# Kernel optimization log

Hardware: AMD Instinct MI355X
Metric: run time of the kernel (lower is better)

## Reference

```python
import jax, jax.numpy as jnp
import numpy as np

N, DIM, K = 262144, 64, 1024

def setup_inputs() -> dict:
    key = jax.random.key(0)
    k1, k2 = jax.random.split(key)
    x = jax.random.normal(k1, (N, DIM), dtype=jnp.float32)
    embed = jax.random.normal(k2, (K, DIM), dtype=jnp.float32)
    return {"x": x, "embed": embed}

def reference(x, embed):
    distances = (jnp.sum(x * x, axis=-1, keepdims=True)
                 - 2.0 * (x @ embed.T)
                 + jnp.sum(embed * embed, axis=-1))  # [N, K]
    idx = jnp.argmin(distances, axis=-1)  # [N]
    # dequantize: embedding lookup
    out = embed[idx]  # [N, DIM]
    return out
```

## Files before the change

kernel.cpp:

```cpp
#include <hip/hip_runtime.h>


#define VQ_N 262144
#define VQ_DIM 64
#define VQ_K 1024
#define NT 64
#define TCH 256
#define FLAG_EPS 1.2e-2f

typedef short short8 __attribute__((ext_vector_type(8)));
typedef float f32x4 __attribute__((ext_vector_type(4)));

#define WS_BFRAG 0
#define WS_E2    (256*1024)
#define WS_NEEDED (260*1024)

static __device__ __forceinline__ unsigned short f2bf_rtne(float f) {
    unsigned u = __float_as_uint(f);
    unsigned r = u + 0x7FFFu + ((u >> 16) & 1u);
    return (unsigned short)(r >> 16);
}
static __device__ __forceinline__ float bf2f(unsigned short h) {
    return __uint_as_float(((unsigned)h) << 16);
}

__global__ void vq_prep(const float* __restrict__ embed, unsigned char* ws) {
    int t = blockIdx.x * 256 + threadIdx.x;
    if (t < NT * TCH) {
        int ct = t >> 8;
        int c = t & 255;
        int arr = c >> 7;
        int kc = (c >> 6) & 1;
        int l = c & 63;
        int code = ct * 16 + (l & 15);
        int kbase = kc * 32 + ((l >> 4) << 3);
        const float* ep = embed + (size_t)code * VQ_DIM + kbase;
        short8 pack;
#pragma unroll
        for (int j = 0; j < 8; ++j) {
            float v = ep[j];
            unsigned short h = f2bf_rtne(v);
            pack[j] = arr ? (short)f2bf_rtne(v - bf2f(h)) : (short)h;
        }
        ((short8*)(ws + WS_BFRAG))[t] = pack;
    } else if (t < NT * TCH + VQ_K) {
        int code = t - NT * TCH;
        const float* ep = embed + (size_t)code * VQ_DIM;
        float a0 = 0, a1 = 0, a2 = 0, a3 = 0;
#pragma unroll
        for (int j = 0; j < VQ_DIM; j += 4) {
            a0 = fmaf(ep[j], ep[j], a0);
            a1 = fmaf(ep[j + 1], ep[j + 1], a1);
            a2 = fmaf(ep[j + 2], ep[j + 2], a2);
            a3 = fmaf(ep[j + 3], ep[j + 3], a3);
        }
        ((float*)(ws + WS_E2))[code] = (a0 + a1) + (a2 + a3);
    }
}

__global__ __launch_bounds__(256, 2)
void vq_stage1(const float* __restrict__ x, const float* __restrict__ embed,
               unsigned char* ws, float* __restrict__ out) {
    __shared__ int idx_s[4][64];

    const int tid = threadIdx.x;
    const int lane = tid & 63;
    const int wave = tid >> 6;
    const int gwave = blockIdx.x * 4 + wave;
    const int R0 = gwave * 64;
    const int g = lane >> 4;
    const int khalf = g << 3;

    const short8* bsrc = (const short8*)(ws + WS_BFRAG);
    const float* e2g = (const float*)(ws + WS_E2);

    short8 ah00, ah01, al00, al01, ah10, ah11, al10, al11;
    short8 ah20, ah21, al20, al21, ah30, ah31, al30, al31;
#define MAKE_A(ROW, KC, AH, AL)                                             \
    {                                                                       \
        const float4* p4 = (const float4*)(x + (size_t)(ROW) * VQ_DIM +     \
                                           (KC) * 32 + khalf);              \
        float4 v0 = p4[0], v1 = p4[1];                                      \
        float q0 = -2.0f * v0.x, q1 = -2.0f * v0.y, q2 = -2.0f * v0.z,      \
              q3 = -2.0f * v0.w, q4 = -2.0f * v1.x, q5 = -2.0f * v1.y,      \
              q6 = -2.0f * v1.z, q7 = -2.0f * v1.w;                         \
        unsigned short h0 = f2bf_rtne(q0), h1 = f2bf_rtne(q1),              \
                       h2 = f2bf_rtne(q2), h3 = f2bf_rtne(q3),              \
                       h4 = f2bf_rtne(q4), h5 = f2bf_rtne(q5),              \
                       h6 = f2bf_rtne(q6), h7 = f2bf_rtne(q7);              \
        AH[0] = (short)h0; AH[1] = (short)h1; AH[2] = (short)h2;            \
        AH[3] = (short)h3; AH[4] = (short)h4; AH[5] = (short)h5;            \
        AH[6] = (short)h6; AH[7] = (short)h7;                               \
        AL[0] = (short)f2bf_rtne(q0 - bf2f(h0));                            \
        AL[1] = (short)f2bf_rtne(q1 - bf2f(h1));                            \
        AL[2] = (short)f2bf_rtne(q2 - bf2f(h2));                            \
        AL[3] = (short)f2bf_rtne(q3 - bf2f(h3));                            \
        AL[4] = (short)f2bf_rtne(q4 - bf2f(h4));                            \
        AL[5] = (short)f2bf_rtne(q5 - bf2f(h5));                            \
        AL[6] = (short)f2bf_rtne(q6 - bf2f(h6));                            \
        AL[7] = (short)f2bf_rtne(q7 - bf2f(h7));                            \
    }
    const int rowb = R0 + (lane & 15);
    MAKE_A(rowb +  0, 0, ah00, al00)  MAKE_A(rowb +  0, 1, ah01, al01)
    MAKE_A(rowb + 16, 0, ah10, al10)  MAKE_A(rowb + 16, 1, ah11, al11)
    MAKE_A(rowb + 32, 0, ah20, al20)  MAKE_A(rowb + 32, 1, ah21, al21)
    MAKE_A(rowb + 48, 0, ah30, al30)  MAKE_A(rowb + 48, 1, ah31, al31)
#undef MAKE_A

    unsigned m1k0[4], m2k0[4], m1k1[4], m2k1[4];
    unsigned m1k2[4], m2k2[4], m1k3[4], m2k3[4];
#pragma unroll
    for (int r = 0; r < 4; ++r) {
        m1k0[r] = 0xFFFFFFFFu; m2k0[r] = 0xFFFFFFFFu;
        m1k1[r] = 0xFFFFFFFFu; m2k1[r] = 0xFFFFFFFFu;
        m1k2[r] = 0xFFFFFFFFu; m2k2[r] = 0xFFFFFFFFu;
        m1k3[r] = 0xFFFFFFFFu; m2k3[r] = 0xFFFFFFFFu;
    }

#define DO_SET(AH0, AH1, AL0, AL1, M1, M2)                                            \
    {                                                                                 \
        f32x4 acc = {e2c, e2c, e2c, e2c};                                             \
        acc = __builtin_amdgcn_mfma_f32_16x16x32_bf16(AL0, bh0, acc, 0, 0, 0);        \
        acc = __builtin_amdgcn_mfma_f32_16x16x32_bf16(AL1, bh1, acc, 0, 0, 0);        \
        acc = __builtin_amdgcn_mfma_f32_16x16x32_bf16(AH0, bl0, acc, 0, 0, 0);        \
        acc = __builtin_amdgcn_mfma_f32_16x16x32_bf16(AH1, bl1, acc, 0, 0, 0);        \
        acc = __builtin_amdgcn_mfma_f32_16x16x32_bf16(AH0, bh0, acc, 0, 0, 0);        \
        acc = __builtin_amdgcn_mfma_f32_16x16x32_bf16(AH1, bh1, acc, 0, 0, 0);        \
        _Pragma("unroll")                                                             \
        for (int r = 0; r < 4; ++r) {                                                 \
            unsigned key = (__float_as_uint(acc[r]) & 0xFFFFFFC0u) | ctu;             \
            unsigned t1 = M1[r] > key ? M1[r] : key;                                  \
            M2[r] = M2[r] < t1 ? M2[r] : t1;                                          \
            M1[r] = M1[r] < key ? M1[r] : key;                                        \
        }                                                                             \
    }

#pragma unroll 2
    for (int ct = 0; ct < NT; ++ct) {
        const short8* bt = bsrc + (size_t)ct * TCH;
        short8 bh0 = bt[lane];
        short8 bh1 = bt[64 + lane];
        short8 bl0 = bt[128 + lane];
        short8 bl1 = bt[192 + lane];
        float e2c = e2g[ct * 16 + (lane & 15)] + 256.0f;
        unsigned ctu = (unsigned)ct;

        DO_SET(ah00, ah01, al00, al01, m1k0, m2k0)
        DO_SET(ah10, ah11, al10, al11, m1k1, m2k1)
        DO_SET(ah20, ah21, al20, al21, m1k2, m2k2)
        DO_SET(ah30, ah31, al30, al31, m1k3, m2k3)
    }
#undef DO_SET

    unsigned res0[4], res1[4], res2[4], res3[4];
#pragma unroll
    for (int r = 0; r < 4; ++r) {
        res0[r] = (unsigned)(lane & 15); res1[r] = res0[r];
        res2[r] = res0[r]; res3[r] = res0[r];
    }
#define RED_STEP(M1, M2, RES, m)                                                      \
    {                                                                                 \
        _Pragma("unroll")                                                             \
        for (int r = 0; r < 4; ++r) {                                                 \
            unsigned ok = (unsigned)__shfl_xor((int)M1[r], m);                        \
            unsigned ok2 = (unsigned)__shfl_xor((int)M2[r], m);                       \
            unsigned orr = (unsigned)__shfl_xor((int)RES[r], m);                      \
            unsigned t1 = M1[r] > ok ? M1[r] : ok;                                    \
            unsigned c2 = ok2 < t1 ? ok2 : t1;                                        \
            M2[r] = M2[r] < c2 ? M2[r] : c2;                                          \
            bool take = (ok < M1[r]) || (ok == M1[r] && orr < RES[r]);                \
            if (take) { M1[r] = ok; RES[r] = orr; }                                   \
        }                                                                             \
    }
#pragma unroll
    for (int m = 1; m <= 8; m <<= 1) {
        RED_STEP(m1k0, m2k0, res0, m)
        RED_STEP(m1k1, m2k1, res1, m)
        RED_STEP(m1k2, m2k2, res2, m)
        RED_STEP(m1k3, m2k3, res3, m)
    }
#undef RED_STEP

    unsigned long long lmask = 0ull;
    if ((lane & 15) == 0) {
#define PUB(M1, M2, RES, SET)                                                         \
        _Pragma("unroll")                                                             \
        for (int r = 0; r < 4; ++r) {                                                 \
            int p = (SET) * 16 + 4 * g + r;                                           \
            idx_s[wave][p] = (int)((M1[r] & 63u) * 16u + RES[r]);                     \
            float s1 = __uint_as_float(M1[r] & 0xFFFFFFC0u);                          \
            float s2 = __uint_as_float(M2[r] & 0xFFFFFFC0u);                          \
            if (s2 - s1 < FLAG_EPS) lmask |= 1ull << p;                               \
        }
        PUB(m1k0, m2k0, res0, 0)
        PUB(m1k1, m2k1, res1, 1)
        PUB(m1k2, m2k2, res2, 2)
        PUB(m1k3, m2k3, res3, 3)
#undef PUB
    }
    lmask |= (unsigned long long)__shfl_xor((long long)lmask, 16);
    lmask |= (unsigned long long)__shfl_xor((long long)lmask, 32);
    unsigned long long wmask = (unsigned long long)__shfl((long long)lmask, 0);
    __syncthreads();

    const int chunk = tid & 15;
#pragma unroll
    for (int jj = 0; jj < 16; ++jj) {
        int rib = jj * 16 + (tid >> 4);
        int code = idx_s[rib >> 6][rib & 63];
        const float4* ep = (const float4*)(embed + (size_t)code * VQ_DIM) + chunk;
        float4* op = (float4*)(out + (size_t)(blockIdx.x * 256 + rib) * VQ_DIM) + chunk;
        *op = *ep;
    }
    __syncthreads();

    while (wmask) {
        int b = __ffsll((unsigned long long)wmask) - 1;
        wmask &= wmask - 1;
        int row = R0 + b;
        const float* xr = x + (size_t)row * VQ_DIM;
        float xv[VQ_DIM];
#pragma unroll
        for (int j = 0; j < VQ_DIM / 4; ++j) {
            float4 v = ((const float4*)xr)[j];
            xv[4 * j] = v.x; xv[4 * j + 1] = v.y;
            xv[4 * j + 2] = v.z; xv[4 * j + 3] = v.w;
        }
        float best = __builtin_inff();
        int bi = VQ_K;
        for (int t = 0; t < VQ_K / 64; ++t) {
            int c = t * 64 + lane;
            const float* ep = embed + (size_t)c * VQ_DIM;
            float a0 = 0, a1 = 0, a2 = 0, a3 = 0;
#pragma unroll
            for (int j = 0; j < VQ_DIM; j += 4) {
                a0 = fmaf(xv[j], ep[j], a0);
                a1 = fmaf(xv[j + 1], ep[j + 1], a1);
                a2 = fmaf(xv[j + 2], ep[j + 2], a2);
                a3 = fmaf(xv[j + 3], ep[j + 3], a3);
            }
            float dot = (a0 + a1) + (a2 + a3);
            float s = fmaf(-2.0f, dot, e2g[c]);
            if (s < best || (s == best && c < bi)) { best = s; bi = c; }
        }
#pragma unroll
        for (int m = 1; m <= 32; m <<= 1) {
            float ob = __shfl_xor(best, m);
            int oi = __shfl_xor(bi, m);
            if (ob < best || (ob == best && oi < bi)) { best = ob; bi = oi; }
        }
        out[(size_t)row * VQ_DIM + lane] = embed[(size_t)bi * VQ_DIM + lane];
    }
}

__global__ __launch_bounds__(256, 4)
void vq_fallback(const float* __restrict__ x, const float* __restrict__ embed,
                 float* __restrict__ out) {
    __shared__ float e2s[VQ_K];
    const int tid = threadIdx.x;
    for (int c = tid; c < VQ_K; c += 256) {
        const float4* ep = (const float4*)(embed + c * VQ_DIM);
        float s = 0.0f;
#pragma unroll
        for (int j = 0; j < VQ_DIM / 4; ++j) {
            float4 v = ep[j];
            s = fmaf(v.x, v.x, s); s = fmaf(v.y, v.y, s);
            s = fmaf(v.z, v.z, s); s = fmaf(v.w, v.w, s);
        }
        e2s[c] = s;
    }
    __syncthreads();
    const int row = blockIdx.x * 256 + tid;
    float xr[VQ_DIM];
    const float4* xp = (const float4*)(x + (size_t)row * VQ_DIM);
#pragma unroll
    for (int j = 0; j < VQ_DIM / 4; ++j) {
        float4 v = xp[j];
        xr[4 * j] = v.x; xr[4 * j + 1] = v.y; xr[4 * j + 2] = v.z; xr[4 * j + 3] = v.w;
    }
    float best = __builtin_inff();
    int bidx = 0;
    for (int c = 0; c < VQ_K; ++c) {
        const float4* ep = (const float4*)(embed + c * VQ_DIM);
        float a0 = 0, a1 = 0, a2 = 0, a3 = 0;
#pragma unroll
        for (int j = 0; j < VQ_DIM / 4; ++j) {
            float4 v = ep[j];
            a0 = fmaf(xr[4 * j], v.x, a0);
            a1 = fmaf(xr[4 * j + 1], v.y, a1);
            a2 = fmaf(xr[4 * j + 2], v.z, a2);
            a3 = fmaf(xr[4 * j + 3], v.w, a3);
        }
        float score = fmaf(-2.0f, (a0 + a1) + (a2 + a3), e2s[c]);
        if (score < best) { best = score; bidx = c; }
    }
    const float4* bp = (const float4*)(embed + (size_t)bidx * VQ_DIM);
    float4* op = (float4*)(out + (size_t)row * VQ_DIM);
#pragma unroll
    for (int j = 0; j < VQ_DIM / 4; ++j) op[j] = bp[j];
}

extern "C" void kernel_launch(void* const* d_in, const int* in_sizes, int n_in,
                              void* d_out, int out_size, void* d_ws, size_t ws_size,
                              hipStream_t stream) {
    const float* x = (const float*)d_in[0];
    const float* embed = (const float*)d_in[1];
    float* out = (float*)d_out;
    if (ws_size < WS_NEEDED) {
        hipLaunchKernelGGL(vq_fallback, dim3(VQ_N / 256), dim3(256), 0, stream, x, embed, out);
        return;
    }
    unsigned char* ws = (unsigned char*)d_ws;
    hipLaunchKernelGGL(vq_prep, dim3(68), dim3(256), 0, stream, embed, ws);
    hipLaunchKernelGGL(vq_stage1, dim3(VQ_N / 256), dim3(256), 0, stream, x, embed, ws, out);
}
```

Before: 183.3 us.

## Halve rows per wave, double occupancy, prefetch codebook tiles with rotated start

```diff
diff --git a/kernel.cpp b/kernel.cpp
--- a/kernel.cpp
+++ b/kernel.cpp
@@ -13,7 +13,8 @@
 
 #define WS_BFRAG 0
 #define WS_E2    (256*1024)
-#define WS_NEEDED (260*1024)
+#define WS_E2P   (260*1024)
+#define WS_NEEDED (264*1024)
 
 static __device__ __forceinline__ unsigned short f2bf_rtne(float f) {
     unsigned u = __float_as_uint(f);
@@ -54,28 +55,30 @@
             a2 = fmaf(ep[j + 2], ep[j + 2], a2);
             a3 = fmaf(ep[j + 3], ep[j + 3], a3);
         }
-        ((float*)(ws + WS_E2))[code] = (a0 + a1) + (a2 + a3);
-    }
-}
-
-__global__ __launch_bounds__(256, 2)
+        float e2 = (a0 + a1) + (a2 + a3);
+        ((float*)(ws + WS_E2))[code] = e2;
+        ((float*)(ws + WS_E2P))[code] = e2 + 256.0f;
+    }
+}
+
+__global__ __launch_bounds__(256, 4)
 void vq_stage1(const float* __restrict__ x, const float* __restrict__ embed,
                unsigned char* ws, float* __restrict__ out) {
-    __shared__ int idx_s[4][64];
+    __shared__ int idx_s[4][32];
 
     const int tid = threadIdx.x;
     const int lane = tid & 63;
     const int wave = tid >> 6;
     const int gwave = blockIdx.x * 4 + wave;
-    const int R0 = gwave * 64;
+    const int R0 = gwave * 32;
     const int g = lane >> 4;
     const int khalf = g << 3;
 
     const short8* bsrc = (const short8*)(ws + WS_BFRAG);
     const float* e2g = (const float*)(ws + WS_E2);
+    const float* e2p = (const float*)(ws + WS_E2P);
 
     short8 ah00, ah01, al00, al01, ah10, ah11, al10, al11;
-    short8 ah20, ah21, al20, al21, ah30, ah31, al30, al31;
 #define MAKE_A(ROW, KC, AH, AL)                                             \
     {                                                                       \
         const float4* p4 = (const float4*)(x + (size_t)(ROW) * VQ_DIM +     \
@@ -100,32 +103,37 @@
         AL[6] = (short)f2bf_rtne(q6 - bf2f(h6));                            \
         AL[7] = (short)f2bf_rtne(q7 - bf2f(h7));                            \
     }
-    const int rowb = R0 + (lane & 15);
-    MAKE_A(rowb +  0, 0, ah00, al00)  MAKE_A(rowb +  0, 1, ah01, al01)
-    MAKE_A(rowb + 16, 0, ah10, al10)  MAKE_A(rowb + 16, 1, ah11, al11)
-    MAKE_A(rowb + 32, 0, ah20, al20)  MAKE_A(rowb + 32, 1, ah21, al21)
-    MAKE_A(rowb + 48, 0, ah30, al30)  MAKE_A(rowb + 48, 1, ah31, al31)
+    const int row0 = R0 + (lane & 15);
+    const int row1 = row0 + 16;
+    MAKE_A(row0, 0, ah00, al00)
+    MAKE_A(row0, 1, ah01, al01)
+    MAKE_A(row1, 0, ah10, al10)
+    MAKE_A(row1, 1, ah11, al11)
 #undef MAKE_A
 
     unsigned m1k0[4], m2k0[4], m1k1[4], m2k1[4];
-    unsigned m1k2[4], m2k2[4], m1k3[4], m2k3[4];
 #pragma unroll
     for (int r = 0; r < 4; ++r) {
         m1k0[r] = 0xFFFFFFFFu; m2k0[r] = 0xFFFFFFFFu;
         m1k1[r] = 0xFFFFFFFFu; m2k1[r] = 0xFFFFFFFFu;
-        m1k2[r] = 0xFFFFFFFFu; m2k2[r] = 0xFFFFFFFFu;
-        m1k3[r] = 0xFFFFFFFFu; m2k3[r] = 0xFFFFFFFFu;
-    }
-
-#define DO_SET(AH0, AH1, AL0, AL1, M1, M2)                                            \
+    }
+
+#define LOAD_B(CT, B0, B1, B2, B3)                                          \
+    {                                                                       \
+        const short8* bt = bsrc + (size_t)(CT) * TCH;                       \
+        B0 = bt[lane]; B1 = bt[64 + lane];                                  \
+        B2 = bt[128 + lane]; B3 = bt[192 + lane];                           \
+    }
+
+#define DO_SET(AH0, AH1, AL0, AL1, B0, B1, B2, B3, M1, M2)                            \
     {                                                                                 \
         f32x4 acc = {e2c, e2c, e2c, e2c};                                             \
-        acc = __builtin_amdgcn_mfma_f32_16x16x32_bf16(AL0, bh0, acc, 0, 0, 0);        \
-        acc = __builtin_amdgcn_mfma_f32_16x16x32_bf16(AL1, bh1, acc, 0, 0, 0);        \
-        acc = __builtin_amdgcn_mfma_f32_16x16x32_bf16(AH0, bl0, acc, 0, 0, 0);        \
-        acc = __builtin_amdgcn_mfma_f32_16x16x32_bf16(AH1, bl1, acc, 0, 0, 0);        \
-        acc = __builtin_amdgcn_mfma_f32_16x16x32_bf16(AH0, bh0, acc, 0, 0, 0);        \
-        acc = __builtin_amdgcn_mfma_f32_16x16x32_bf16(AH1, bh1, acc, 0, 0, 0);        \
+        acc = __builtin_amdgcn_mfma_f32_16x16x32_bf16(AL0, B0, acc, 0, 0, 0);         \
+        acc = __builtin_amdgcn_mfma_f32_16x16x32_bf16(AL1, B1, acc, 0, 0, 0);         \
+        acc = __builtin_amdgcn_mfma_f32_16x16x32_bf16(AH0, B2, acc, 0, 0, 0);         \
+        acc = __builtin_amdgcn_mfma_f32_16x16x32_bf16(AH1, B3, acc, 0, 0, 0);         \
+        acc = __builtin_amdgcn_mfma_f32_16x16x32_bf16(AH0, B0, acc, 0, 0, 0);         \
+        acc = __builtin_amdgcn_mfma_f32_16x16x32_bf16(AH1, B1, acc, 0, 0, 0);         \
         _Pragma("unroll")                                                             \
         for (int r = 0; r < 4; ++r) {                                                 \
             unsigned key = (__float_as_uint(acc[r]) & 0xFFFFFFC0u) | ctu;             \
@@ -135,29 +143,33 @@
         }                                                                             \
     }
 
-#pragma unroll 2
-    for (int ct = 0; ct < NT; ++ct) {
-        const short8* bt = bsrc + (size_t)ct * TCH;
-        short8 bh0 = bt[lane];
-        short8 bh1 = bt[64 + lane];
-        short8 bl0 = bt[128 + lane];
-        short8 bl1 = bt[192 + lane];
-        float e2c = e2g[ct * 16 + (lane & 15)] + 256.0f;
-        unsigned ctu = (unsigned)ct;
-
-        DO_SET(ah00, ah01, al00, al01, m1k0, m2k0)
-        DO_SET(ah10, ah11, al10, al11, m1k1, m2k1)
-        DO_SET(ah20, ah21, al20, al21, m1k2, m2k2)
-        DO_SET(ah30, ah31, al30, al31, m1k3, m2k3)
-    }
+#define DO_TILE(CT, B0, B1, B2, B3)                                                   \
+    {                                                                                 \
+        float e2c = e2p[(CT) * 16 + (lane & 15)];                                     \
+        unsigned ctu = (unsigned)(CT);                                                \
+        DO_SET(ah00, ah01, al00, al01, B0, B1, B2, B3, m1k0, m2k0)                    \
+        DO_SET(ah10, ah11, al10, al11, B0, B1, B2, B3, m1k1, m2k1)                    \
+    }
+
+    const int rot = gwave & 63;
+    short8 pb0, pb1, pb2, pb3, qb0, qb1, qb2, qb3;
+    LOAD_B(rot, pb0, pb1, pb2, pb3)
+    for (int it = 0; it < NT; it += 2) {
+        const int cte = (rot + it) & 63;
+        const int cto = (rot + it + 1) & 63;
+        const int ctn = (rot + it + 2) & 63;
+        LOAD_B(cto, qb0, qb1, qb2, qb3)
+        DO_TILE(cte, pb0, pb1, pb2, pb3)
+        LOAD_B(ctn, pb0, pb1, pb2, pb3)
+        DO_TILE(cto, qb0, qb1, qb2, qb3)
+    }
+#undef DO_TILE
 #undef DO_SET
-
-    unsigned res0[4], res1[4], res2[4], res3[4];
-#pragma unroll
-    for (int r = 0; r < 4; ++r) {
-        res0[r] = (unsigned)(lane & 15); res1[r] = res0[r];
-        res2[r] = res0[r]; res3[r] = res0[r];
-    }
+#undef LOAD_B
+
+    unsigned res0[4], res1[4];
+#pragma unroll
+    for (int r = 0; r < 4; ++r) { res0[r] = (unsigned)(lane & 15); res1[r] = res0[r]; }
 #define RED_STEP(M1, M2, RES, m)                                                      \
     {                                                                                 \
         _Pragma("unroll")                                                             \
@@ -176,46 +188,41 @@
     for (int m = 1; m <= 8; m <<= 1) {
         RED_STEP(m1k0, m2k0, res0, m)
         RED_STEP(m1k1, m2k1, res1, m)
-        RED_STEP(m1k2, m2k2, res2, m)
-        RED_STEP(m1k3, m2k3, res3, m)
     }
 #undef RED_STEP
 
-    unsigned long long lmask = 0ull;
+    unsigned fmask = 0;
     if ((lane & 15) == 0) {
-#define PUB(M1, M2, RES, SET)                                                         \
-        _Pragma("unroll")                                                             \
-        for (int r = 0; r < 4; ++r) {                                                 \
-            int p = (SET) * 16 + 4 * g + r;                                           \
-            idx_s[wave][p] = (int)((M1[r] & 63u) * 16u + RES[r]);                     \
-            float s1 = __uint_as_float(M1[r] & 0xFFFFFFC0u);                          \
-            float s2 = __uint_as_float(M2[r] & 0xFFFFFFC0u);                          \
-            if (s2 - s1 < FLAG_EPS) lmask |= 1ull << p;                               \
-        }
-        PUB(m1k0, m2k0, res0, 0)
-        PUB(m1k1, m2k1, res1, 1)
-        PUB(m1k2, m2k2, res2, 2)
-        PUB(m1k3, m2k3, res3, 3)
-#undef PUB
-    }
-    lmask |= (unsigned long long)__shfl_xor((long long)lmask, 16);
-    lmask |= (unsigned long long)__shfl_xor((long long)lmask, 32);
-    unsigned long long wmask = (unsigned long long)__shfl((long long)lmask, 0);
+#pragma unroll
+        for (int r = 0; r < 4; ++r) {
+            int rl0 = 4 * g + r;
+            idx_s[wave][rl0] = (int)((m1k0[r] & 63u) * 16u + res0[r]);
+            float s1 = __uint_as_float(m1k0[r] & 0xFFFFFFC0u);
+            float s2 = __uint_as_float(m2k0[r] & 0xFFFFFFC0u);
+            if (s2 - s1 < FLAG_EPS) fmask |= 1u << rl0;
+            int rl1 = 16 + 4 * g + r;
+            idx_s[wave][rl1] = (int)((m1k1[r] & 63u) * 16u + res1[r]);
+            float t1f = __uint_as_float(m1k1[r] & 0xFFFFFFC0u);
+            float t2f = __uint_as_float(m2k1[r] & 0xFFFFFFC0u);
+            if (t2f - t1f < FLAG_EPS) fmask |= 1u << rl1;
+        }
+    }
+    fmask |= (unsigned)__shfl_xor((int)fmask, 16);
+    fmask |= (unsigned)__shfl_xor((int)fmask, 32);
+    unsigned wmask = (unsigned)__shfl((int)fmask, 0);
     __syncthreads();
 
-    const int chunk = tid & 15;
-#pragma unroll
-    for (int jj = 0; jj < 16; ++jj) {
-        int rib = jj * 16 + (tid >> 4);
-        int code = idx_s[rib >> 6][rib & 63];
-        const float4* ep = (const float4*)(embed + (size_t)code * VQ_DIM) + chunk;
-        float4* op = (float4*)(out + (size_t)(blockIdx.x * 256 + rib) * VQ_DIM) + chunk;
-        *op = *ep;
-    }
+    const int orow = tid >> 1;
+    const int ohalf = tid & 1;
+    int code = idx_s[orow >> 5][orow & 31];
+    const float4* ep = (const float4*)(embed + (size_t)code * VQ_DIM) + ohalf * 8;
+    float4* op = (float4*)(out + (size_t)(blockIdx.x * 128 + orow) * VQ_DIM) + ohalf * 8;
+#pragma unroll
+    for (int j = 0; j < 8; ++j) op[j] = ep[j];
     __syncthreads();
 
     while (wmask) {
-        int b = __ffsll((unsigned long long)wmask) - 1;
+        int b = __ffs(wmask) - 1;
         wmask &= wmask - 1;
         int row = R0 + b;
         const float* xr = x + (size_t)row * VQ_DIM;
@@ -230,14 +237,14 @@
         int bi = VQ_K;
         for (int t = 0; t < VQ_K / 64; ++t) {
             int c = t * 64 + lane;
-            const float* ep = embed + (size_t)c * VQ_DIM;
+            const float* ep2 = embed + (size_t)c * VQ_DIM;
             float a0 = 0, a1 = 0, a2 = 0, a3 = 0;
 #pragma unroll
             for (int j = 0; j < VQ_DIM; j += 4) {
-                a0 = fmaf(xv[j], ep[j], a0);
-                a1 = fmaf(xv[j + 1], ep[j + 1], a1);
-                a2 = fmaf(xv[j + 2], ep[j + 2], a2);
-                a3 = fmaf(xv[j + 3], ep[j + 3], a3);
+                a0 = fmaf(xv[j], ep2[j], a0);
+                a1 = fmaf(xv[j + 1], ep2[j + 1], a1);
+                a2 = fmaf(xv[j + 2], ep2[j + 2], a2);
+                a3 = fmaf(xv[j + 3], ep2[j + 3], a3);
             }
             float dot = (a0 + a1) + (a2 + a3);
             float s = fmaf(-2.0f, dot, e2g[c]);
@@ -312,5 +319,5 @@
     }
     unsigned char* ws = (unsigned char*)d_ws;
     hipLaunchKernelGGL(vq_prep, dim3(68), dim3(256), 0, stream, embed, ws);
-    hipLaunchKernelGGL(vq_stage1, dim3(VQ_N / 256), dim3(256), 0, stream, x, embed, ws, out);
-}
+    hipLaunchKernelGGL(vq_stage1, dim3(VQ_N / 128), dim3(256), 0, stream, x, embed, ws, out);
+}
```

Result: faster. 172.8 us (-5.7%).
